# Optimization experiments

Hardware: AMD Instinct MI355X
Metric: run time of the kernel (lower is better)

## Reference

```python
import jax, jax.numpy as jnp
import numpy as np

N_NODES = 100000


def _gcn_conv(x, edge_index, W, b, n_nodes):
    # PyG GCNConv: add self-loops, symmetric normalization, linear, aggregate, bias.
    src, dst = edge_index[0], edge_index[1]
    loop = jnp.arange(n_nodes, dtype=src.dtype)
    src = jnp.concatenate([src, loop])
    dst = jnp.concatenate([dst, loop])
    deg = jax.ops.segment_sum(jnp.ones_like(dst, dtype=x.dtype), dst, num_segments=n_nodes)
    dinv = jax.lax.rsqrt(jnp.maximum(deg, 1.0))  # deg >= 1 due to self-loops
    norm = dinv[src] * dinv[dst]                 # [E+N]
    h = x @ W                                    # [N, out]
    msg = h[src] * norm[:, None]                 # [E+N, out] gather
    out = jax.ops.segment_sum(msg, dst, num_segments=n_nodes)  # scatter-add
    return out + b


def setup_inputs() -> dict:
    key = jax.random.key(0)
    k1, k2, k3, k4, k5 = jax.random.split(key, 5)
    in_c, hid = 128, 64
    x = jax.random.normal(k1, (N_NODES, in_c), dtype=jnp.float32)
    edge_index = jax.random.randint(k2, (2, 1600000), 0, N_NODES, dtype=jnp.int64)
    s1 = 1.0 / np.sqrt(in_c)
    s2 = 1.0 / np.sqrt(2 * hid)
    W1 = jax.random.uniform(k3, (in_c, 2 * hid), jnp.float32, -s1, s1)
    b1 = jnp.zeros((2 * hid,), jnp.float32)
    W2 = jax.random.uniform(k4, (2 * hid, hid), jnp.float32, -s2, s2)
    b2 = jnp.zeros((hid,), jnp.float32)
    return {"x": x, "edge_index": edge_index, "W1": W1, "b1": b1, "W2": W2, "b2": b2}


def reference(x, edge_index, W1, b1, W2, b2):
    h = jax.nn.relu(_gcn_conv(x, edge_index, W1, b1, N_NODES))
    return _gcn_conv(h, edge_index, W2, b2, N_NODES)
```

## Files before the change

kernel.cpp:

```cpp
#include <hip/hip_runtime.h>
#include <hip/hip_fp16.h>
#include <cstdint>

constexpr int K_IN = 128;
constexpr int N_H1 = 128;
constexpr int N_H2 = 64;

constexpr int NPR      = 128;
constexpr int NREG_PAD = 800;
constexpr int BCHUNKS  = 256;
constexpr int RCAP     = 2560;

typedef _Float16 half8 __attribute__((ext_vector_type(8)));
typedef _Float16 half4 __attribute__((ext_vector_type(4)));
typedef float    f32x4 __attribute__((ext_vector_type(4)));

__device__ __forceinline__ void acc_h8(float* acc, uint4 u) {
    const __half2* h = (const __half2*)&u;
    #pragma unroll
    for (int i = 0; i < 4; ++i) {
        float2 f = __half22float2(h[i]);
        acc[2 * i]     += f.x;
        acc[2 * i + 1] += f.y;
    }
}
__device__ __forceinline__ void init_h8(float* acc, uint4 u) {
    const __half2* h = (const __half2*)&u;
    #pragma unroll
    for (int i = 0; i < 4; ++i) {
        float2 f = __half22float2(h[i]);
        acc[2 * i]     = f.x;
        acc[2 * i + 1] = f.y;
    }
}
__device__ __forceinline__ void store_h4(__half* p, float4 v) {
    __half2 a = __floats2half2_rn(v.x, v.y), b = __floats2half2_rn(v.z, v.w);
    uint2 u;
    u.x = *(unsigned*)&a; u.y = *(unsigned*)&b;
    *(uint2*)p = u;
}


__launch_bounds__(256)
__global__ void hist_kernel(const int* __restrict__ dst, int* __restrict__ hist,
                            int E, int nreg, int chunk) {
    __shared__ int h[NREG_PAD];
    const int tid = threadIdx.x, b = blockIdx.x;
    for (int i = tid; i < nreg; i += 256) h[i] = 0;
    __syncthreads();
    const int lo = b * chunk, hi = min(lo + chunk, E);
    for (int i = lo + tid; i < hi; i += 256) atomicAdd(&h[dst[i] >> 7], 1);
    __syncthreads();
    for (int i = tid; i < nreg; i += 256) hist[(long)b * nreg + i] = h[i];
}


__launch_bounds__(BCHUNKS)
__global__ void rscan_kernel(int* __restrict__ hist, int* __restrict__ totals, int nreg) {
    __shared__ int sh[BCHUNKS];
    const int r = blockIdx.x, t = threadIdx.x;
    int v = hist[(long)t * nreg + r];
    sh[t] = v;
    __syncthreads();
    #pragma unroll
    for (int off = 1; off < BCHUNKS; off <<= 1) {
        int u = (t >= off) ? sh[t - off] : 0;
        __syncthreads();
        sh[t] += u;
        __syncthreads();
    }
    hist[(long)t * nreg + r] = sh[t] - v;
    if (t == BCHUNKS - 1) totals[r] = sh[t];
}


__launch_bounds__(256)
__global__ void scatter_kernel(const int* __restrict__ src, const int* __restrict__ dst,
                               const int* __restrict__ hist,
                               int* __restrict__ pedge, int E, int nreg, int chunk) {
    __shared__ int cur[NREG_PAD];
    const int tid = threadIdx.x, b = blockIdx.x;
    for (int i = tid; i < nreg; i += 256)
        cur[i] = hist[(long)b * nreg + i];
    __syncthreads();
    const int lo = b * chunk, hi = min(lo + chunk, E);
    for (int i = lo + tid; i < hi; i += 256) {
        int d = dst[i];
        int r = d >> 7;
        int p = atomicAdd(&cur[r], 1);
        if (p < RCAP)
            pedge[(long)r * RCAP + p] = ((d & (NPR - 1)) << 17) | src[i];
    }
}


__launch_bounds__(256)
__global__ void csr_build_kernel(const int* __restrict__ totals,
                                 const int* __restrict__ pedge,
                                 int* __restrict__ pos, int* __restrict__ cnt,
                                 float* __restrict__ dinv, int* __restrict__ ssrc, int n) {
    __shared__ int cnt_l[NPR];
    __shared__ int scan_l[NPR];
    __shared__ int pos_mut[NPR];

    const int r   = blockIdx.x;
    const int tid = threadIdx.x;
    const long wb = (long)r * RCAP;
    const int ne  = min(totals[r], RCAP);

    if (tid < NPR) cnt_l[tid] = 0;
    __syncthreads();

    const int* pe = &pedge[wb];
    for (int j = tid; j < ne; j += 256) atomicAdd(&cnt_l[pe[j] >> 17], 1);
    __syncthreads();

    if (tid < NPR) scan_l[tid] = cnt_l[tid];
    __syncthreads();
    #pragma unroll
    for (int off = 1; off < NPR; off <<= 1) {
        int v = (tid < NPR && tid >= off) ? scan_l[tid - off] : 0;
        __syncthreads();
        if (tid < NPR) scan_l[tid] += v;
        __syncthreads();
    }
    if (tid < NPR) {
        int excl = scan_l[tid] - cnt_l[tid];
        pos_mut[tid] = excl;
        int node = r * NPR + tid;
        if (node < n) {
            pos[node]  = (int)wb + excl;
            cnt[node]  = cnt_l[tid];
            dinv[node] = rsqrtf((float)cnt_l[tid] + 1.0f);
        }
    }
    __syncthreads();

    int* so = &ssrc[wb];
    for (int j = tid; j < ne; j += 256) {
        int v = pe[j];
        int p = atomicAdd(&pos_mut[v >> 17], 1);
        so[p] = v & 0x1FFFF;
    }
}


__launch_bounds__(256)
__global__ void gemm1_mfma_kernel(const float* __restrict__ X, const float* __restrict__ W,
                                  const float* __restrict__ dinv,
                                  __half* __restrict__ H, int nrows) {
    __shared__ __align__(16) _Float16 Wt[128 * 136];
    __shared__ __align__(16) _Float16 xh[64 * 136];

    const int tid  = threadIdx.x;
    const long row0 = (long)blockIdx.x * 64;

    #pragma unroll 4
    for (int i = 0; i < 64; ++i) {
        int flat = tid + i * 256;
        int k    = flat >> 7;
        int col  = flat & 127;
        Wt[col * 136 + k] = (_Float16)W[k * 128 + col];
    }

    #pragma unroll
    for (int i = 0; i < 32; ++i) {
        int flat = tid + i * 256;
        int row  = flat >> 5;
        int c4   = flat & 31;
        long grow = row0 + row;
        if (grow >= nrows) grow = nrows - 1;
        float4 v = *(const float4*)&X[grow * 128 + c4 * 4];
        half4 hv = { (_Float16)v.x, (_Float16)v.y, (_Float16)v.z, (_Float16)v.w };
        *(half4*)&xh[row * 136 + c4 * 4] = hv;
    }
    __syncthreads();

    const int w    = tid >> 6;
    const int lane = tid & 63;
    const int lr   = lane & 15;
    const int loct = lane >> 4;

    half8 afrag[4];
    #pragma unroll
    for (int kt = 0; kt < 4; ++kt)
        afrag[kt] = *(const half8*)&xh[(16 * w + lr) * 136 + kt * 32 + loct * 8];

    float dv[4];
    #pragma unroll
    for (int reg = 0; reg < 4; ++reg) {
        long grow = row0 + 16 * w + (lane >> 4) * 4 + reg;
        dv[reg] = (grow < nrows) ? dinv[grow] : 0.f;
    }

    #pragma unroll
    for (int ct = 0; ct < 8; ++ct) {
        f32x4 acc = {0.f, 0.f, 0.f, 0.f};
        #pragma unroll
        for (int kt = 0; kt < 4; ++kt) {
            half8 b = *(const half8*)&Wt[(ct * 16 + lr) * 136 + kt * 32 + loct * 8];
            acc = __builtin_amdgcn_mfma_f32_16x16x32_f16(afrag[kt], b, acc, 0, 0, 0);
        }
        const int gcol = ct * 16 + lr;
        #pragma unroll
        for (int reg = 0; reg < 4; ++reg) {
            long grow = row0 + 16 * w + (lane >> 4) * 4 + reg;
            if (grow < nrows)
                H[grow * 128 + gcol] = __float2half(acc[reg] * dv[reg]);
        }
    }
}


__launch_bounds__(256)
__global__ void fused_l2_kernel(const int* __restrict__ pos, const int* __restrict__ cnt,
                                const int* __restrict__ ssrc,
                                const float* __restrict__ dinv, const __half* __restrict__ h1h,
                                const float* __restrict__ b1, const float* __restrict__ W2,
                                __half* __restrict__ h2h, int n) {
    __shared__ float qs[16][132];

    const int tid  = threadIdx.x;
    const int g    = tid >> 4;
    const int sub  = tid & 15;
    const int base = blockIdx.x * 16;

    {
        int node = base + g;
        if (node < n) {
            int deg = cnt[node];
            const int* bu = &ssrc[pos[node]];
            float acc[8];
            init_h8(acc, *(const uint4*)&h1h[(long)node * 128 + sub * 8]);
            int j = 0;
            for (; j + 3 < deg; j += 4) {
                int s0 = bu[j], s1 = bu[j + 1], s2 = bu[j + 2], s3 = bu[j + 3];
                uint4 v0 = *(const uint4*)&h1h[(long)s0 * 128 + sub * 8];
                uint4 v1 = *(const uint4*)&h1h[(long)s1 * 128 + sub * 8];
                uint4 v2 = *(const uint4*)&h1h[(long)s2 * 128 + sub * 8];
                uint4 v3 = *(const uint4*)&h1h[(long)s3 * 128 + sub * 8];
                acc_h8(acc, v0); acc_h8(acc, v1); acc_h8(acc, v2); acc_h8(acc, v3);
            }
            for (; j < deg; ++j) {
                uint4 v = *(const uint4*)&h1h[(long)bu[j] * 128 + sub * 8];
                acc_h8(acc, v);
            }
            float dvn = dinv[node];
            float4 ba = *(const float4*)&b1[sub * 8];
            float4 bb = *(const float4*)&b1[sub * 8 + 4];
            float4 q0, q1;
            q0.x = fmaxf(dvn * (dvn * acc[0] + ba.x), 0.f);
            q0.y = fmaxf(dvn * (dvn * acc[1] + ba.y), 0.f);
            q0.z = fmaxf(dvn * (dvn * acc[2] + ba.z), 0.f);
            q0.w = fmaxf(dvn * (dvn * acc[3] + ba.w), 0.f);
            q1.x = fmaxf(dvn * (dvn * acc[4] + bb.x), 0.f);
            q1.y = fmaxf(dvn * (dvn * acc[5] + bb.y), 0.f);
            q1.z = fmaxf(dvn * (dvn * acc[6] + bb.z), 0.f);
            q1.w = fmaxf(dvn * (dvn * acc[7] + bb.w), 0.f);
            *(float4*)&qs[g][sub * 8]     = q0;
            *(float4*)&qs[g][sub * 8 + 4] = q1;
        }
    }
    __syncthreads();

    {
        const int bn = tid >> 4;
        const int c4 = tid & 15;
        int node = base + bn;
        if (node < n) {
            float4 acc = {0.f, 0.f, 0.f, 0.f};
            #pragma unroll 4
            for (int k0 = 0; k0 < 128; k0 += 4) {
                float4 q4 = *(const float4*)&qs[bn][k0];
                float qk[4] = {q4.x, q4.y, q4.z, q4.w};
                #pragma unroll
                for (int kk = 0; kk < 4; ++kk) {
                    float4 wv = *(const float4*)&W2[(k0 + kk) * 64 + c4 * 4];
                    acc.x += qk[kk] * wv.x; acc.y += qk[kk] * wv.y;
                    acc.z += qk[kk] * wv.z; acc.w += qk[kk] * wv.w;
                }
            }
            store_h4(&h2h[(long)node * 64 + c4 * 4], acc);
        }
    }
}


__launch_bounds__(256)
__global__ void agg2_kernel(const int* __restrict__ pos, const int* __restrict__ cnt,
                            const int* __restrict__ ssrc,
                            const float* __restrict__ dinv, const __half* __restrict__ Hs,
                            const float* __restrict__ bias, float* __restrict__ OUT, int n) {
    const int tid  = threadIdx.x;
    const int node = blockIdx.x * 32 + (tid >> 3);
    const int sub  = tid & 7;
    if (node >= n) return;

    int deg = cnt[node];
    const int* bu = &ssrc[pos[node]];

    float acc[8];
    init_h8(acc, *(const uint4*)&Hs[(long)node * 64 + sub * 8]);
    int j = 0;
    for (; j + 3 < deg; j += 4) {
        int s0 = bu[j], s1 = bu[j + 1], s2 = bu[j + 2], s3 = bu[j + 3];
        uint4 v0 = *(const uint4*)&Hs[(long)s0 * 64 + sub * 8];
        uint4 v1 = *(const uint4*)&Hs[(long)s1 * 64 + sub * 8];
        uint4 v2 = *(const uint4*)&Hs[(long)s2 * 64 + sub * 8];
        uint4 v3 = *(const uint4*)&Hs[(long)s3 * 64 + sub * 8];
        acc_h8(acc, v0); acc_h8(acc, v1); acc_h8(acc, v2); acc_h8(acc, v3);
    }
    for (; j < deg; ++j) {
        uint4 v = *(const uint4*)&Hs[(long)bu[j] * 64 + sub * 8];
        acc_h8(acc, v);
    }

    const float d = dinv[node];
    float4 ba = *(const float4*)&bias[sub * 8];
    float4 bb = *(const float4*)&bias[sub * 8 + 4];
    float4 o0 = { acc[0] * d + ba.x, acc[1] * d + ba.y,
                  acc[2] * d + ba.z, acc[3] * d + ba.w };
    float4 o1 = { acc[4] * d + bb.x, acc[5] * d + bb.y,
                  acc[6] * d + bb.z, acc[7] * d + bb.w };
    *(float4*)&OUT[(long)node * 64 + sub * 8]     = o0;
    *(float4*)&OUT[(long)node * 64 + sub * 8 + 4] = o1;
}


extern "C" void kernel_launch(void* const* d_in, const int* in_sizes, int n_in,
                              void* d_out, int out_size, void* d_ws, size_t ws_size,
                              hipStream_t stream) {
    const float* x   = (const float*)d_in[0];
    const int*   ei  = (const int*)d_in[1];
    const float* W1  = (const float*)d_in[2];
    const float* b1  = (const float*)d_in[3];
    const float* W2  = (const float*)d_in[4];
    const float* b2  = (const float*)d_in[5];
    float*       out = (float*)d_out;

    const int N = in_sizes[0] / K_IN;
    const int E = in_sizes[1] / 2;

    const int* esrc = ei;
    const int* edst = ei + E;

    const int NREG  = (N + NPR - 1) / NPR;
    const int CHUNK = (E + BCHUNKS - 1) / BCHUNKS;

    char*   ws     = (char*)d_ws;
    int*    hist   = (int*)ws;
    int*    totals = hist + (size_t)BCHUNKS * NREG;
    int*    pos    = totals + NREG_PAD;
    int*    cnt    = pos + N;
    float*  dinv   = (float*)(cnt + N);
    int*    pedge  = (int*)(dinv + N);
    int*    ssrc   = pedge + (size_t)NREG * RCAP;
    __half* h1h    = (__half*)(ssrc + (size_t)NREG * RCAP);
    __half* h2h    = h1h + (size_t)N * N_H1;

    hist_kernel<<<BCHUNKS, 256, 0, stream>>>(edst, hist, E, NREG, CHUNK);
    rscan_kernel<<<NREG, BCHUNKS, 0, stream>>>(hist, totals, NREG);
    scatter_kernel<<<BCHUNKS, 256, 0, stream>>>(esrc, edst, hist, pedge, E, NREG, CHUNK);
    csr_build_kernel<<<NREG, 256, 0, stream>>>(totals, pedge, pos, cnt, dinv, ssrc, N);

    gemm1_mfma_kernel<<<(N + 63) / 64, 256, 0, stream>>>(x, W1, dinv, h1h, N);

    fused_l2_kernel<<<(N + 15) / 16, 256, 0, stream>>>(pos, cnt, ssrc, dinv, h1h, b1, W2, h2h, N);

    agg2_kernel<<<(N + 31) / 32, 256, 0, stream>>>(pos, cnt, ssrc, dinv, h2h, b2, out, N);
}
```

Before: 262.3 us.

## Merge histogram, scan and scatter into one pass with global atomic region cursors

Replaces the three-kernel hist/region-scan/scatter bucketing with a single kernel. Each block counts its edges per region in shared memory, reserves space in each region with one global atomicAdd, then scatters its edges. This removes two launches and the per-block histogram round trip. The cost is that edge order within a region is no longer deterministic. It also halves the number of chunk blocks and unrolls the gather loops in both aggregation kernels to 8 loads in flight.

```diff
diff --git a/kernel.cpp b/kernel.cpp
--- a/kernel.cpp
+++ b/kernel.cpp
@@ -8,7 +8,7 @@
 
 constexpr int NPR      = 128;
 constexpr int NREG_PAD = 800;
-constexpr int BCHUNKS  = 256;
+constexpr int BCHUNKS  = 128;
 constexpr int RCAP     = 2560;
 
 typedef _Float16 half8 __attribute__((ext_vector_type(8)));
@@ -40,54 +40,37 @@
     *(uint2*)p = u;
 }
 
-
-__launch_bounds__(256)
-__global__ void hist_kernel(const int* __restrict__ dst, int* __restrict__ hist,
-                            int E, int nreg, int chunk) {
-    __shared__ int h[NREG_PAD];
+__global__ void zero_int_kernel(int* __restrict__ p, int n) {
+    int i = blockIdx.x * blockDim.x + threadIdx.x;
+    if (i < n) p[i] = 0;
+}
+
+
+__launch_bounds__(256)
+__global__ void scatter1p_kernel(const int* __restrict__ src, const int* __restrict__ dst,
+                                 int* __restrict__ gcur, int* __restrict__ pedge,
+                                 int E, int nreg, int chunk) {
+    __shared__ int cnt_l[NREG_PAD];
+    __shared__ int cur_l[NREG_PAD];
     const int tid = threadIdx.x, b = blockIdx.x;
-    for (int i = tid; i < nreg; i += 256) h[i] = 0;
-    __syncthreads();
     const int lo = b * chunk, hi = min(lo + chunk, E);
-    for (int i = lo + tid; i < hi; i += 256) atomicAdd(&h[dst[i] >> 7], 1);
-    __syncthreads();
-    for (int i = tid; i < nreg; i += 256) hist[(long)b * nreg + i] = h[i];
-}
-
-
-__launch_bounds__(BCHUNKS)
-__global__ void rscan_kernel(int* __restrict__ hist, int* __restrict__ totals, int nreg) {
-    __shared__ int sh[BCHUNKS];
-    const int r = blockIdx.x, t = threadIdx.x;
-    int v = hist[(long)t * nreg + r];
-    sh[t] = v;
-    __syncthreads();
-    #pragma unroll
-    for (int off = 1; off < BCHUNKS; off <<= 1) {
-        int u = (t >= off) ? sh[t - off] : 0;
-        __syncthreads();
-        sh[t] += u;
-        __syncthreads();
-    }
-    hist[(long)t * nreg + r] = sh[t] - v;
-    if (t == BCHUNKS - 1) totals[r] = sh[t];
-}
-
-
-__launch_bounds__(256)
-__global__ void scatter_kernel(const int* __restrict__ src, const int* __restrict__ dst,
-                               const int* __restrict__ hist,
-                               int* __restrict__ pedge, int E, int nreg, int chunk) {
-    __shared__ int cur[NREG_PAD];
-    const int tid = threadIdx.x, b = blockIdx.x;
-    for (int i = tid; i < nreg; i += 256)
-        cur[i] = hist[(long)b * nreg + i];
-    __syncthreads();
-    const int lo = b * chunk, hi = min(lo + chunk, E);
+
+    for (int i = tid; i < nreg; i += 256) cnt_l[i] = 0;
+    __syncthreads();
+
+    for (int i = lo + tid; i < hi; i += 256) atomicAdd(&cnt_l[dst[i] >> 7], 1);
+    __syncthreads();
+
+    for (int i = tid; i < nreg; i += 256) {
+        int c = cnt_l[i];
+        cur_l[i] = (c > 0) ? atomicAdd(&gcur[i], c) : 0;
+    }
+    __syncthreads();
+
     for (int i = lo + tid; i < hi; i += 256) {
         int d = dst[i];
         int r = d >> 7;
-        int p = atomicAdd(&cur[r], 1);
+        int p = atomicAdd(&cur_l[r], 1);
         if (p < RCAP)
             pedge[(long)r * RCAP + p] = ((d & (NPR - 1)) << 17) | src[i];
     }
@@ -95,7 +78,7 @@
 
 
 __launch_bounds__(256)
-__global__ void csr_build_kernel(const int* __restrict__ totals,
+__global__ void csr_build_kernel(const int* __restrict__ gcur,
                                  const int* __restrict__ pedge,
                                  int* __restrict__ pos, int* __restrict__ cnt,
                                  float* __restrict__ dinv, int* __restrict__ ssrc, int n) {
@@ -106,7 +89,7 @@
     const int r   = blockIdx.x;
     const int tid = threadIdx.x;
     const long wb = (long)r * RCAP;
-    const int ne  = min(totals[r], RCAP);
+    const int ne  = min(gcur[r], RCAP);
 
     if (tid < NPR) cnt_l[tid] = 0;
     __syncthreads();
@@ -233,12 +216,23 @@
             float acc[8];
             init_h8(acc, *(const uint4*)&h1h[(long)node * 128 + sub * 8]);
             int j = 0;
+            for (; j + 7 < deg; j += 8) {
+                uint4 v0 = *(const uint4*)&h1h[(long)bu[j + 0] * 128 + sub * 8];
+                uint4 v1 = *(const uint4*)&h1h[(long)bu[j + 1] * 128 + sub * 8];
+                uint4 v2 = *(const uint4*)&h1h[(long)bu[j + 2] * 128 + sub * 8];
+                uint4 v3 = *(const uint4*)&h1h[(long)bu[j + 3] * 128 + sub * 8];
+                uint4 v4 = *(const uint4*)&h1h[(long)bu[j + 4] * 128 + sub * 8];
+                uint4 v5 = *(const uint4*)&h1h[(long)bu[j + 5] * 128 + sub * 8];
+                uint4 v6 = *(const uint4*)&h1h[(long)bu[j + 6] * 128 + sub * 8];
+                uint4 v7 = *(const uint4*)&h1h[(long)bu[j + 7] * 128 + sub * 8];
+                acc_h8(acc, v0); acc_h8(acc, v1); acc_h8(acc, v2); acc_h8(acc, v3);
+                acc_h8(acc, v4); acc_h8(acc, v5); acc_h8(acc, v6); acc_h8(acc, v7);
+            }
             for (; j + 3 < deg; j += 4) {
-                int s0 = bu[j], s1 = bu[j + 1], s2 = bu[j + 2], s3 = bu[j + 3];
-                uint4 v0 = *(const uint4*)&h1h[(long)s0 * 128 + sub * 8];
-                uint4 v1 = *(const uint4*)&h1h[(long)s1 * 128 + sub * 8];
-                uint4 v2 = *(const uint4*)&h1h[(long)s2 * 128 + sub * 8];
-                uint4 v3 = *(const uint4*)&h1h[(long)s3 * 128 + sub * 8];
+                uint4 v0 = *(const uint4*)&h1h[(long)bu[j + 0] * 128 + sub * 8];
+                uint4 v1 = *(const uint4*)&h1h[(long)bu[j + 1] * 128 + sub * 8];
+                uint4 v2 = *(const uint4*)&h1h[(long)bu[j + 2] * 128 + sub * 8];
+                uint4 v3 = *(const uint4*)&h1h[(long)bu[j + 3] * 128 + sub * 8];
                 acc_h8(acc, v0); acc_h8(acc, v1); acc_h8(acc, v2); acc_h8(acc, v3);
             }
             for (; j < deg; ++j) {
@@ -302,12 +296,23 @@
     float acc[8];
     init_h8(acc, *(const uint4*)&Hs[(long)node * 64 + sub * 8]);
     int j = 0;
+    for (; j + 7 < deg; j += 8) {
+        uint4 v0 = *(const uint4*)&Hs[(long)bu[j + 0] * 64 + sub * 8];
+        uint4 v1 = *(const uint4*)&Hs[(long)bu[j + 1] * 64 + sub * 8];
+        uint4 v2 = *(const uint4*)&Hs[(long)bu[j + 2] * 64 + sub * 8];
+        uint4 v3 = *(const uint4*)&Hs[(long)bu[j + 3] * 64 + sub * 8];
+        uint4 v4 = *(const uint4*)&Hs[(long)bu[j + 4] * 64 + sub * 8];
+        uint4 v5 = *(const uint4*)&Hs[(long)bu[j + 5] * 64 + sub * 8];
+        uint4 v6 = *(const uint4*)&Hs[(long)bu[j + 6] * 64 + sub * 8];
+        uint4 v7 = *(const uint4*)&Hs[(long)bu[j + 7] * 64 + sub * 8];
+        acc_h8(acc, v0); acc_h8(acc, v1); acc_h8(acc, v2); acc_h8(acc, v3);
+        acc_h8(acc, v4); acc_h8(acc, v5); acc_h8(acc, v6); acc_h8(acc, v7);
+    }
     for (; j + 3 < deg; j += 4) {
-        int s0 = bu[j], s1 = bu[j + 1], s2 = bu[j + 2], s3 = bu[j + 3];
-        uint4 v0 = *(const uint4*)&Hs[(long)s0 * 64 + sub * 8];
-        uint4 v1 = *(const uint4*)&Hs[(long)s1 * 64 + sub * 8];
-        uint4 v2 = *(const uint4*)&Hs[(long)s2 * 64 + sub * 8];
-        uint4 v3 = *(const uint4*)&Hs[(long)s3 * 64 + sub * 8];
+        uint4 v0 = *(const uint4*)&Hs[(long)bu[j + 0] * 64 + sub * 8];
+        uint4 v1 = *(const uint4*)&Hs[(long)bu[j + 1] * 64 + sub * 8];
+        uint4 v2 = *(const uint4*)&Hs[(long)bu[j + 2] * 64 + sub * 8];
+        uint4 v3 = *(const uint4*)&Hs[(long)bu[j + 3] * 64 + sub * 8];
         acc_h8(acc, v0); acc_h8(acc, v1); acc_h8(acc, v2); acc_h8(acc, v3);
     }
     for (; j < deg; ++j) {
@@ -348,9 +353,8 @@
     const int CHUNK = (E + BCHUNKS - 1) / BCHUNKS;
 
     char*   ws     = (char*)d_ws;
-    int*    hist   = (int*)ws;
-    int*    totals = hist + (size_t)BCHUNKS * NREG;
-    int*    pos    = totals + NREG_PAD;
+    int*    gcur   = (int*)ws;
+    int*    pos    = gcur + NREG_PAD;
     int*    cnt    = pos + N;
     float*  dinv   = (float*)(cnt + N);
     int*    pedge  = (int*)(dinv + N);
@@ -358,10 +362,9 @@
     __half* h1h    = (__half*)(ssrc + (size_t)NREG * RCAP);
     __half* h2h    = h1h + (size_t)N * N_H1;
 
-    hist_kernel<<<BCHUNKS, 256, 0, stream>>>(edst, hist, E, NREG, CHUNK);
-    rscan_kernel<<<NREG, BCHUNKS, 0, stream>>>(hist, totals, NREG);
-    scatter_kernel<<<BCHUNKS, 256, 0, stream>>>(esrc, edst, hist, pedge, E, NREG, CHUNK);
-    csr_build_kernel<<<NREG, 256, 0, stream>>>(totals, pedge, pos, cnt, dinv, ssrc, N);
+    zero_int_kernel<<<(NREG + 255) / 256, 256, 0, stream>>>(gcur, NREG);
+    scatter1p_kernel<<<BCHUNKS, 256, 0, stream>>>(esrc, edst, gcur, pedge, E, NREG, CHUNK);
+    csr_build_kernel<<<NREG, 256, 0, stream>>>(gcur, pedge, pos, cnt, dinv, ssrc, N);
 
     gemm1_mfma_kernel<<<(N + 63) / 64, 256, 0, stream>>>(x, W1, dinv, h1h, N);
 
```

New measurement: 280.0 us. 6.7% more time.
